# Kernel tuning notes

Hardware: AMD Instinct MI355X
Metric: run time of the kernel (lower is better)

Reference implementation:

```python
import jax, jax.numpy as jnp
import numpy as np

B, T, C = 8, 1024, 576
NH, NKV = 9, 3          # query heads, kv heads
HD = C // NH            # 64 head dim
KVC = C // NKV          # 192 kv proj width
N_REP = NH // NKV       # 3


def setup_inputs() -> dict:
    key = jax.random.key(0)
    ks = jax.random.split(key, 9)
    s = 0.02
    return {
        "x": jax.random.normal(ks[0], (B, T, C), jnp.float32),
        "Wq": jax.random.normal(ks[1], (C, C), jnp.float32) * s,
        "bq": jax.random.normal(ks[2], (C,), jnp.float32) * s,
        "Wk": jax.random.normal(ks[3], (C, KVC), jnp.float32) * s,
        "bk": jax.random.normal(ks[4], (KVC,), jnp.float32) * s,
        "Wv": jax.random.normal(ks[5], (C, KVC), jnp.float32) * s,
        "bv": jax.random.normal(ks[6], (KVC,), jnp.float32) * s,
        "Wo": jax.random.normal(ks[7], (C, C), jnp.float32) * s,
        "bo": jax.random.normal(ks[8], (C,), jnp.float32) * s,
    }


def reference(x, Wq, bq, Wk, bk, Wv, bv, Wo, bo):
    Bx, Tx, Cx = x.shape
    q = x @ Wq + bq                                # [B,T,C]
    k = x @ Wk + bk                                # [B,T,KVC]
    v = x @ Wv + bv
    # split heads: q -> [B,NH,T,HD]; k,v -> [B,NKV,T,HD]
    q = q.reshape(Bx, Tx, NH, HD).transpose(0, 2, 1, 3)
    k = k.reshape(Bx, Tx, NKV, HD).transpose(0, 2, 1, 3)
    v = v.reshape(Bx, Tx, NKV, HD).transpose(0, 2, 1, 3)
    # repeat_kv: [B,NKV,T,HD] -> [B,NKV*N_REP,T,HD]
    k = jnp.repeat(k, N_REP, axis=1)
    v = jnp.repeat(v, N_REP, axis=1)
    att = jnp.einsum("bhqd,bhkd->bhqk", q, k) * (1.0 / np.sqrt(HD))
    mask = jnp.tril(jnp.ones((Tx, Tx), bool))
    att = jnp.where(mask, att, -jnp.inf)
    att = jax.nn.softmax(att, axis=-1)
    y = jnp.einsum("bhqk,bhkd->bhqd", att, v)      # [B,NH,T,HD]
    y = y.transpose(0, 2, 1, 3).reshape(Bx, Tx, Cx)
    return y @ Wo + bo
```

## Files before the change

kernel.cpp:

```cpp
#include <hip/hip_runtime.h>
#include <hip/hip_bf16.h>
#include <math.h>

#define B_    8
#define T_    1024
#define C_    576
#define NH_   9
#define NKV_  3
#define HD_   64
#define KVC_  192
#define NREP_ 3
#define NQKV_ 960
#define NTK_  9

typedef __attribute__((ext_vector_type(8))) short bf16x8;
typedef __attribute__((ext_vector_type(4))) float f32x4;
typedef __attribute__((ext_vector_type(4))) int i32x4;

#define MFMA_16x16x32(a, b, c) __builtin_amdgcn_mfma_f32_16x16x32_bf16((a), (b), (c), 0, 0, 0)

__device__ __forceinline__ ushort f2bf(float f) {
  __hip_bfloat16 h = __float2bfloat16(f);
  return *reinterpret_cast<const ushort*>(&h);
}

__device__ __forceinline__ float fexp2(float x) { return __builtin_amdgcn_exp2f(x); }

__device__ __forceinline__ int swz(int row, int col) {
  int byte = (row << 7) + (col << 1);
  return (byte ^ ((row & 7) << 4)) >> 1;
}

__device__ __forceinline__ void gload16(const ushort* g, ushort* l) {
  __builtin_amdgcn_global_load_lds(
      (const __attribute__((address_space(1))) unsigned int*)g,
      (__attribute__((address_space(3))) unsigned int*)l, 16, 0, 0);
}

__device__ __forceinline__ i32x4 packrow(const float* src) {
  const float4 a = *reinterpret_cast<const float4*>(src);
  const float4 b = *reinterpret_cast<const float4*>(src + 4);
  union { ushort u[8]; i32x4 v; } t;
  t.u[0] = f2bf(a.x); t.u[1] = f2bf(a.y); t.u[2] = f2bf(a.z); t.u[3] = f2bf(a.w);
  t.u[4] = f2bf(b.x); t.u[5] = f2bf(b.y); t.u[6] = f2bf(b.z); t.u[7] = f2bf(b.w);
  return t.v;
}

__global__ __launch_bounds__(256) void convert_x_kernel(
    const float* __restrict__ x, ushort* __restrict__ xbt) {
  const int tm = blockIdx.x, tk = blockIdx.y;
  ushort* dst = xbt + ((size_t)tm * NTK_ + tk) * 8192;
  #pragma unroll
  for (int i = 0; i < 4; i++) {
    const int c = threadIdx.x + i * 256;
    const int row = c >> 3, colb = (c & 7) * 8;
    *reinterpret_cast<i32x4*>(&dst[swz(row, colb)]) =
        packrow(x + (size_t)(tm * 128 + row) * C_ + tk * 64 + colb);
  }
}

__global__ __launch_bounds__(256) void convert_w_kernel(
    const float* __restrict__ Wq, const float* __restrict__ Wk,
    const float* __restrict__ Wv, const float* __restrict__ Wo,
    const float* __restrict__ bq, const float* __restrict__ bk,
    const float* __restrict__ bv, const float* __restrict__ bo,
    ushort* __restrict__ wqkvT, ushort* __restrict__ woT, float* __restrict__ bcat) {
  const int tnc = blockIdx.x, tk = blockIdx.y;
  #pragma unroll
  for (int i = 0; i < 2; i++) {
    const int c = threadIdx.x + i * 256;
    const int row = c >> 3, colb = (c & 7) * 8;
    const float* src; int ld; ushort* dst; int ncol;
    if (tnc < 15) {
      const int n = tnc * 64 + row;
      if (n < 576)      { src = Wq; ld = C_;  ncol = n; }
      else if (n < 768) { src = Wk; ld = KVC_; ncol = n - 576; }
      else              { src = Wv; ld = KVC_; ncol = n - 768; }
      dst = wqkvT + ((size_t)tnc * NTK_ + tk) * 4096;
    } else {
      src = Wo; ld = C_; ncol = (tnc - 15) * 64 + row;
      dst = woT + ((size_t)(tnc - 15) * NTK_ + tk) * 4096;
    }
    union { ushort u[8]; i32x4 v; } t;
    #pragma unroll
    for (int e = 0; e < 8; e++)
      t.u[e] = f2bf(src[(size_t)(tk * 64 + colb + e) * ld + ncol]);
    *reinterpret_cast<i32x4*>(&dst[swz(row, colb)]) = t.v;
    if (tk == 0 && (c & 7) == 0) {
      const int n = tnc * 64 + row;
      float bv_;
      if (n < 576)       bv_ = bq[n];
      else if (n < 768)  bv_ = bk[n - 576];
      else if (n < 960)  bv_ = bv[n - 768];
      else               bv_ = bo[n - 960];
      bcat[n] = bv_;
    }
  }
}

template<int MODE>
__global__ __launch_bounds__(256) void gemm_lds_kernel(
    const ushort* __restrict__ At, const ushort* __restrict__ Bt,
    const float* __restrict__ bias, void* __restrict__ Cp,
    ushort* __restrict__ ktv, ushort* __restrict__ vtv, int N) {
  const int nwg = gridDim.x * gridDim.y;
  const int flat = blockIdx.y * gridDim.x + blockIdx.x;
  const int wg = (flat & 7) * (nwg >> 3) + (flat >> 3);
  const int bxs = wg % gridDim.x, bys = wg / gridDim.x;

  __shared__ ushort As[128 * 64];
  __shared__ ushort Bs[64 * 64];
  const int bm = bys * 128, bn = bxs * 64;
  const int tid = threadIdx.x;
  const int wave = tid >> 6, lane = tid & 63;
  const int lg = lane >> 4, ll = lane & 15;
  const int wm = (wave >> 1) * 64, wn = (wave & 1) * 32;
  f32x4 acc[4][2] = {};

  const ushort* abase = At + (size_t)bys * NTK_ * 8192;
  const ushort* bbase = Bt + (size_t)bxs * NTK_ * 4096;

  for (int kt = 0; kt < NTK_; kt++) {
    const ushort* ak = abase + (size_t)kt * 8192;
    const ushort* bk = bbase + (size_t)kt * 4096;
    #pragma unroll
    for (int i = 0; i < 4; i++) {
      const int c0 = (wave << 6) + (i << 8);
      gload16(ak + (size_t)(c0 + lane) * 8, &As[c0 * 8]);
    }
    #pragma unroll
    for (int i = 0; i < 2; i++) {
      const int c0 = (wave << 6) + (i << 8);
      gload16(bk + (size_t)(c0 + lane) * 8, &Bs[c0 * 8]);
    }
    __syncthreads();

    bf16x8 af[4][2], bfr[2][2];
    #pragma unroll
    for (int mt = 0; mt < 4; mt++) {
      af[mt][0] = *reinterpret_cast<const bf16x8*>(&As[swz(wm + mt * 16 + ll, lg * 8)]);
      af[mt][1] = *reinterpret_cast<const bf16x8*>(&As[swz(wm + mt * 16 + ll, 32 + lg * 8)]);
    }
    #pragma unroll
    for (int nt = 0; nt < 2; nt++) {
      bfr[nt][0] = *reinterpret_cast<const bf16x8*>(&Bs[swz(wn + nt * 16 + ll, lg * 8)]);
      bfr[nt][1] = *reinterpret_cast<const bf16x8*>(&Bs[swz(wn + nt * 16 + ll, 32 + lg * 8)]);
    }
    #pragma unroll
    for (int mt = 0; mt < 4; mt++) {
      #pragma unroll
      for (int nt = 0; nt < 2; nt++) {
        acc[mt][nt] = MFMA_16x16x32(af[mt][0], bfr[nt][0], acc[mt][nt]);
        acc[mt][nt] = MFMA_16x16x32(af[mt][1], bfr[nt][1], acc[mt][nt]);
      }
    }
    __syncthreads();
  }

  #pragma unroll
  for (int mt = 0; mt < 4; mt++) {
    #pragma unroll
    for (int nt = 0; nt < 2; nt++) {
      const int col = bn + wn + nt * 16 + ll;
      #pragma unroll
      for (int r = 0; r < 4; r++) {
        const int row = bm + wm + mt * 16 + lg * 4 + r;
        const float val = acc[mt][nt][r] + bias[col];
        if (MODE == 0) {
          ((float*)Cp)[(size_t)row * N + col] = val;
        } else {
          if (col < 576) {
            ((ushort*)Cp)[(size_t)row * C_ + col] = f2bf(val * 0.18033688011112042f);
          } else if (col < 768) {
            const int kvh = (col - 576) >> 6, d = (col - 576) & 63;
            ushort* t = ktv + (((size_t)(row >> 10) * 3 + kvh) * 16 + ((row >> 6) & 15)) * 4096;
            t[swz(row & 63, d)] = f2bf(val);
          } else {
            const int kvh = (col - 768) >> 6, d = (col - 768) & 63;
            ushort* t = vtv + (((size_t)(row >> 10) * 3 + kvh) * 16 + ((row >> 6) & 15)) * 4096;
            t[swz(d, row & 63)] = f2bf(val);
          }
        }
      }
    }
  }
}

__global__ __launch_bounds__(256) void attn_mfma_kernel(
    const ushort* __restrict__ qb, const ushort* __restrict__ ktv,
    const ushort* __restrict__ vtv, ushort* __restrict__ yt) {
  const int qt = 15 - blockIdx.z, h = blockIdx.x, b = blockIdx.y;
  const int kvh = h / NREP_;
  const int tid = threadIdx.x;
  const int wave = tid >> 6, lane = tid & 63;
  const int lg = lane >> 4, ll = lane & 15;
  const int w16 = wave << 4;
  const int qrow0 = qt << 6;
  const int nk = (qt + 2) >> 1;

  __shared__ ushort Ks[2][4096];
  __shared__ ushort Vts[2][4096];
  __shared__ ushort Ps[4][1024];

  const ushort* ktb = ktv + ((size_t)b * 3 + kvh) * 16 * 4096;
  const ushort* vtb = vtv + ((size_t)b * 3 + kvh) * 16 * 4096;

  const ushort* qrow = qb + (size_t)(b * T_ + qrow0 + w16 + ll) * C_ + h * HD_;
  const bf16x8 qa0 = *reinterpret_cast<const bf16x8*>(qrow + lg * 8);
  const bf16x8 qa1 = *reinterpret_cast<const bf16x8*>(qrow + 32 + lg * 8);

  f32x4 o[4] = {};
  float m_i = -INFINITY, l_i = 0.f;

  #pragma unroll 1
  for (int kt = 0; kt < nk; kt++) {
    #pragma unroll
    for (int sub = 0; sub < 2; sub++) {
      const ushort* ks = ktb + (size_t)(2 * kt + sub) * 4096;
      const ushort* vs = vtb + (size_t)(2 * kt + sub) * 4096;
      #pragma unroll
      for (int i = 0; i < 2; i++) {
        const int c0 = (wave << 6) + (i << 8);
        gload16(ks + (size_t)(c0 + lane) * 8, &Ks[sub][c0 * 8]);
        gload16(vs + (size_t)(c0 + lane) * 8, &Vts[sub][c0 * 8]);
      }
    }
    __syncthreads();

    f32x4 s[8];
    #pragma unroll
    for (int kc = 0; kc < 8; kc++) {
      const int sub = kc >> 2, kcl = kc & 3;
      const bf16x8 kb0 = *reinterpret_cast<const bf16x8*>(&Ks[sub][swz(kcl * 16 + ll, lg * 8)]);
      const bf16x8 kb1 = *reinterpret_cast<const bf16x8*>(&Ks[sub][swz(kcl * 16 + ll, 32 + lg * 8)]);
      f32x4 z = {};
      z = MFMA_16x16x32(kb0, qa0, z);
      s[kc] = MFMA_16x16x32(kb1, qa1, z);
    }

    if (kt == nk - 1) {
      const int qg = qrow0 + w16 + ll - (kt << 7);
      #pragma unroll
      for (int kc = 0; kc < 8; kc++)
        #pragma unroll
        for (int r = 0; r < 4; r++)
          if (kc * 16 + lg * 4 + r > qg) s[kc][r] = -INFINITY;
    }

    float mA[8];
    #pragma unroll
    for (int kc = 0; kc < 8; kc++)
      mA[kc] = fmaxf(fmaxf(s[kc][0], s[kc][1]), fmaxf(s[kc][2], s[kc][3]));
    float t0 = fmaxf(fmaxf(fmaxf(mA[0], mA[1]), fmaxf(mA[2], mA[3])),
                     fmaxf(fmaxf(mA[4], mA[5]), fmaxf(mA[6], mA[7])));
    t0 = fmaxf(t0, __shfl_xor(t0, 16));
    t0 = fmaxf(t0, __shfl_xor(t0, 32));
    if (!__all(t0 <= m_i + 11.5415603f)) {
      const float mn = fmaxf(m_i, t0);
      const float al = fexp2(m_i - mn);
      m_i = mn;
      l_i *= al;
      #pragma unroll
      for (int r = 0; r < 4; r++) {
        const float ar = __shfl(al, lg * 4 + r);
        o[0][r] *= ar; o[1][r] *= ar; o[2][r] *= ar; o[3][r] *= ar;
      }
    }

    float rsub[2];
    ushort* Pw = Ps[wave];
    #pragma unroll
    for (int sub = 0; sub < 2; sub++) {
      float rk[4];
      #pragma unroll
      for (int kcl = 0; kcl < 4; kcl++) {
        const int kc = sub * 4 + kcl;
        float p0 = fexp2(s[kc][0] - m_i);
        float p1 = fexp2(s[kc][1] - m_i);
        float p2 = fexp2(s[kc][2] - m_i);
        float p3 = fexp2(s[kc][3] - m_i);
        rk[kcl] = (p0 + p1) + (p2 + p3);
        uint w01 = (uint)f2bf(p0) | ((uint)f2bf(p1) << 16);
        uint w23 = (uint)f2bf(p2) | ((uint)f2bf(p3) << 16);
        *reinterpret_cast<uint*>(&Pw[swz(ll, kcl * 16 + lg * 4)])     = w01;
        *reinterpret_cast<uint*>(&Pw[swz(ll, kcl * 16 + lg * 4 + 2)]) = w23;
      }
      rsub[sub] = (rk[0] + rk[1]) + (rk[2] + rk[3]);
      #pragma unroll
      for (int khl = 0; khl < 2; khl++) {
        const bf16x8 pa = *reinterpret_cast<const bf16x8*>(&Pw[swz(ll, khl * 32 + lg * 8)]);
        #pragma unroll
        for (int d0 = 0; d0 < 4; d0++) {
          const bf16x8 vbr = *reinterpret_cast<const bf16x8*>(&Vts[sub][swz(d0 * 16 + ll, khl * 32 + lg * 8)]);
          o[d0] = MFMA_16x16x32(pa, vbr, o[d0]);
        }
      }
    }
    float rs = rsub[0] + rsub[1];
    rs += __shfl_xor(rs, 16);
    rs += __shfl_xor(rs, 32);
    l_i += rs;

    __syncthreads();
  }

  #pragma unroll
  for (int r = 0; r < 4; r++) {
    const float lr = __shfl(l_i, lg * 4 + r);
    const float inv = 1.f / lr;
    const int rowg = b * T_ + qrow0 + w16 + lg * 4 + r;
    ushort* ybase = yt + ((size_t)(rowg >> 7) * NTK_ + h) * 8192;
    const int lrow = rowg & 127;
    #pragma unroll
    for (int d0 = 0; d0 < 4; d0++) {
      ybase[swz(lrow, d0 * 16 + ll)] = f2bf(o[d0][r] * inv);
    }
  }
}

extern "C" void kernel_launch(void* const* d_in, const int* in_sizes, int n_in,
                              void* d_out, int out_size, void* d_ws, size_t ws_size,
                              hipStream_t stream) {
  const float* x  = (const float*)d_in[0];
  const float* Wq = (const float*)d_in[1];
  const float* bq = (const float*)d_in[2];
  const float* Wk = (const float*)d_in[3];
  const float* bk = (const float*)d_in[4];
  const float* Wv = (const float*)d_in[5];
  const float* bv = (const float*)d_in[6];
  const float* Wo = (const float*)d_in[7];
  const float* bo = (const float*)d_in[8];
  float* out = (float*)d_out;

  const int M = B_ * T_;
  ushort* wqkvT = (ushort*)d_ws;
  ushort* woT   = wqkvT + (size_t)15 * NTK_ * 4096;
  float*  bcat  = (float*)(woT + (size_t)9 * NTK_ * 4096);
  ushort* qb    = (ushort*)(bcat + 1536);
  ushort* ktv   = qb + (size_t)M * C_;
  ushort* vtv   = ktv + (size_t)B_ * NKV_ * 16 * 4096;
  ushort* yt    = vtv + (size_t)B_ * NKV_ * 16 * 4096;
  ushort* xbt   = yt + (size_t)M * C_;

  convert_w_kernel<<<dim3(24, NTK_), 256, 0, stream>>>(Wq, Wk, Wv, Wo, bq, bk, bv, bo,
                                                       wqkvT, woT, bcat);
  convert_x_kernel<<<dim3(M / 128, NTK_), 256, 0, stream>>>(x, xbt);
  gemm_lds_kernel<1><<<dim3(NQKV_ / 64, M / 128), 256, 0, stream>>>(
      xbt, wqkvT, bcat, qb, ktv, vtv, NQKV_);
  attn_mfma_kernel<<<dim3(NH_, B_, 16), 256, 0, stream>>>(qb, ktv, vtv, yt);
  gemm_lds_kernel<0><<<dim3(C_ / 64, M / 128), 256, 0, stream>>>(
      yt, woT, bcat + NQKV_, out, nullptr, nullptr, C_);
}
```

Measured before the change: 72.32 us.

## Split long causal query tiles across two blocks and merge partials

The eight longest causal query tiles (qt 8..15) now have their key range split in half across two blocks each. Each half writes unnormalized fp32 partial outputs plus the running max and sum to a workspace buffer. A new merge kernel combines each pair with log-sum-exp rescaling into the bf16 output. The goal is to balance the causal workload and shorten the critical path of the attention kernel. The cost is an extra kernel launch, fp32 partial traffic, and a dependence on the workspace being large enough.

```diff
diff --git a/kernel.cpp b/kernel.cpp
--- a/kernel.cpp
+++ b/kernel.cpp
@@ -188,15 +188,29 @@
 
 __global__ __launch_bounds__(256) void attn_mfma_kernel(
     const ushort* __restrict__ qb, const ushort* __restrict__ ktv,
-    const ushort* __restrict__ vtv, ushort* __restrict__ yt) {
-  const int qt = 15 - blockIdx.z, h = blockIdx.x, b = blockIdx.y;
+    const ushort* __restrict__ vtv, ushort* __restrict__ yt,
+    float* __restrict__ opart) {
+  const int h = blockIdx.x, b = blockIdx.y, bz = blockIdx.z;
+  int qt, kt0, kt1;
+  bool split;
+  if (bz < 16) {
+    qt = 15 - (bz >> 1);
+    const int nk = (qt + 2) >> 1, cA = (nk + 1) >> 1;
+    kt0 = (bz & 1) ? cA : 0;
+    kt1 = (bz & 1) ? nk : cA;
+    split = true;
+  } else {
+    qt = 23 - bz;
+    kt0 = 0; kt1 = (qt + 2) >> 1;
+    split = false;
+  }
+  const int nk_last = ((qt + 2) >> 1) - 1;
   const int kvh = h / NREP_;
   const int tid = threadIdx.x;
   const int wave = tid >> 6, lane = tid & 63;
   const int lg = lane >> 4, ll = lane & 15;
   const int w16 = wave << 4;
   const int qrow0 = qt << 6;
-  const int nk = (qt + 2) >> 1;
 
   __shared__ ushort Ks[2][4096];
   __shared__ ushort Vts[2][4096];
@@ -213,7 +227,7 @@
   float m_i = -INFINITY, l_i = 0.f;
 
   #pragma unroll 1
-  for (int kt = 0; kt < nk; kt++) {
+  for (int kt = kt0; kt < kt1; kt++) {
     #pragma unroll
     for (int sub = 0; sub < 2; sub++) {
       const ushort* ks = ktb + (size_t)(2 * kt + sub) * 4096;
@@ -238,7 +252,7 @@
       s[kc] = MFMA_16x16x32(kb1, qa1, z);
     }
 
-    if (kt == nk - 1) {
+    if (kt == nk_last) {
       const int qg = qrow0 + w16 + ll - (kt << 7);
       #pragma unroll
       for (int kc = 0; kc < 8; kc++)
@@ -304,17 +318,64 @@
     __syncthreads();
   }
 
+  if (!split) {
+    #pragma unroll
+    for (int r = 0; r < 4; r++) {
+      const float lr = __shfl(l_i, lg * 4 + r);
+      const float inv = 1.f / lr;
+      const int rowg = b * T_ + qrow0 + w16 + lg * 4 + r;
+      ushort* ybase = yt + ((size_t)(rowg >> 7) * NTK_ + h) * 8192;
+      const int lrow = rowg & 127;
+      #pragma unroll
+      for (int d0 = 0; d0 < 4; d0++) {
+        ybase[swz(lrow, d0 * 16 + ll)] = f2bf(o[d0][r] * inv);
+      }
+    }
+  } else {
+    float* op = opart + ((size_t)(h * B_ + b) * 16 + bz) * 4224;
+    #pragma unroll
+    for (int r = 0; r < 4; r++) {
+      const int row = w16 + lg * 4 + r;
+      #pragma unroll
+      for (int d0 = 0; d0 < 4; d0++) {
+        op[row * 64 + d0 * 16 + ll] = o[d0][r];
+      }
+    }
+    if (lg == 0) {
+      op[4096 + w16 + ll] = m_i;
+      op[4160 + w16 + ll] = l_i;
+    }
+  }
+}
+
+__global__ __launch_bounds__(256) void attn_merge_kernel(
+    const float* __restrict__ opart, ushort* __restrict__ yt) {
+  const int h = blockIdx.x, b = blockIdx.y, qt = 8 + blockIdx.z;
+  const int tid = threadIdx.x;
+  const int row = tid >> 2, cb = (tid & 3) * 16;
+  const float* p0 = opart + ((size_t)(h * B_ + b) * 16 + (15 - qt) * 2) * 4224;
+  const float* p1 = p0 + 4224;
+
+  const float m0 = p0[4096 + row], m1 = p1[4096 + row];
+  const float l0 = p0[4160 + row], l1 = p1[4160 + row];
+  const float mf = fmaxf(m0, m1);
+  const float a0 = fexp2(m0 - mf), a1 = fexp2(m1 - mf);
+  const float inv = 1.f / (l0 * a0 + l1 * a1);
+
+  const int rowg = b * T_ + (qt << 6) + row;
+  ushort* ybase = yt + ((size_t)(rowg >> 7) * NTK_ + h) * 8192;
+  const int lrow = rowg & 127;
+
   #pragma unroll
-  for (int r = 0; r < 4; r++) {
-    const float lr = __shfl(l_i, lg * 4 + r);
-    const float inv = 1.f / lr;
-    const int rowg = b * T_ + qrow0 + w16 + lg * 4 + r;
-    ushort* ybase = yt + ((size_t)(rowg >> 7) * NTK_ + h) * 8192;
-    const int lrow = rowg & 127;
-    #pragma unroll
-    for (int d0 = 0; d0 < 4; d0++) {
-      ybase[swz(lrow, d0 * 16 + ll)] = f2bf(o[d0][r] * inv);
-    }
+  for (int half = 0; half < 2; half++) {
+    const int c0 = cb + half * 8;
+    union { ushort u[8]; i32x4 v; } t;
+    #pragma unroll
+    for (int e = 0; e < 8; e++) {
+      const float v = (p0[row * 64 + c0 + e] * a0 + p1[row * 64 + c0 + e] * a1) * inv;
+      t.u[e] = f2bf(v);
+    }
+    *reinterpret_cast<i32x4*>(&ybase[swz(lrow, c0)]) = t.v;
   }
 }
 
@@ -341,13 +402,15 @@
   ushort* vtv   = ktv + (size_t)B_ * NKV_ * 16 * 4096;
   ushort* yt    = vtv + (size_t)B_ * NKV_ * 16 * 4096;
   ushort* xbt   = yt + (size_t)M * C_;
+  float*  opart = (float*)(xbt + (size_t)M * C_);
 
   convert_w_kernel<<<dim3(24, NTK_), 256, 0, stream>>>(Wq, Wk, Wv, Wo, bq, bk, bv, bo,
                                                        wqkvT, woT, bcat);
   convert_x_kernel<<<dim3(M / 128, NTK_), 256, 0, stream>>>(x, xbt);
   gemm_lds_kernel<1><<<dim3(NQKV_ / 64, M / 128), 256, 0, stream>>>(
       xbt, wqkvT, bcat, qb, ktv, vtv, NQKV_);
-  attn_mfma_kernel<<<dim3(NH_, B_, 16), 256, 0, stream>>>(qb, ktv, vtv, yt);
+  attn_mfma_kernel<<<dim3(NH_, B_, 24), 256, 0, stream>>>(qb, ktv, vtv, yt, opart);
+  attn_merge_kernel<<<dim3(NH_, B_, 8), 256, 0, stream>>>(opart, yt);
   gemm_lds_kernel<0><<<dim3(C_ / 64, M / 128), 256, 0, stream>>>(
       yt, woT, bcat + NQKV_, out, nullptr, nullptr, C_);
 }
```

Measured after the change: 77.09 us. +6.6%, slower.

## Double-buffer 64-key K/V tiles with async prefetch in attention loop

Applied to the files above, without the earlier changes.

The attention loop now walks 64-key tiles instead of 128-key pairs. It prefetches the next tile's K and V into the alternate LDS buffer while computing on the current one, using an explicit vmcnt wait and raw s_barrier instead of __syncthreads. The finer tile granularity also skips the fully masked half tile on the causal diagonal. The cost is twice as many loop iterations, which means more barriers and more online-softmax rescale checks per key. There is also some dependence on the vmcnt count matching the number of outstanding loads.

```diff
diff --git a/kernel.cpp b/kernel.cpp
--- a/kernel.cpp
+++ b/kernel.cpp
@@ -196,7 +196,7 @@
   const int lg = lane >> 4, ll = lane & 15;
   const int w16 = wave << 4;
   const int qrow0 = qt << 6;
-  const int nk = (qt + 2) >> 1;
+  const int ntile = qt + 1;
 
   __shared__ ushort Ks[2][4096];
   __shared__ ushort Vts[2][4096];
@@ -212,47 +212,59 @@
   f32x4 o[4] = {};
   float m_i = -INFINITY, l_i = 0.f;
 
+  {
+    const ushort* ks = ktb;
+    const ushort* vs = vtb;
+    #pragma unroll
+    for (int i = 0; i < 2; i++) {
+      const int c0 = (wave << 6) + (i << 8);
+      gload16(ks + (size_t)(c0 + lane) * 8, &Ks[0][c0 * 8]);
+      gload16(vs + (size_t)(c0 + lane) * 8, &Vts[0][c0 * 8]);
+    }
+  }
+
   #pragma unroll 1
-  for (int kt = 0; kt < nk; kt++) {
-    #pragma unroll
-    for (int sub = 0; sub < 2; sub++) {
-      const ushort* ks = ktb + (size_t)(2 * kt + sub) * 4096;
-      const ushort* vs = vtb + (size_t)(2 * kt + sub) * 4096;
+  for (int t = 0; t < ntile; t++) {
+    const int cur = t & 1;
+    if (t + 1 < ntile) {
+      const ushort* ks = ktb + (size_t)(t + 1) * 4096;
+      const ushort* vs = vtb + (size_t)(t + 1) * 4096;
       #pragma unroll
       for (int i = 0; i < 2; i++) {
         const int c0 = (wave << 6) + (i << 8);
-        gload16(ks + (size_t)(c0 + lane) * 8, &Ks[sub][c0 * 8]);
-        gload16(vs + (size_t)(c0 + lane) * 8, &Vts[sub][c0 * 8]);
-      }
-    }
-    __syncthreads();
-
-    f32x4 s[8];
-    #pragma unroll
-    for (int kc = 0; kc < 8; kc++) {
-      const int sub = kc >> 2, kcl = kc & 3;
-      const bf16x8 kb0 = *reinterpret_cast<const bf16x8*>(&Ks[sub][swz(kcl * 16 + ll, lg * 8)]);
-      const bf16x8 kb1 = *reinterpret_cast<const bf16x8*>(&Ks[sub][swz(kcl * 16 + ll, 32 + lg * 8)]);
+        gload16(ks + (size_t)(c0 + lane) * 8, &Ks[cur ^ 1][c0 * 8]);
+        gload16(vs + (size_t)(c0 + lane) * 8, &Vts[cur ^ 1][c0 * 8]);
+      }
+      asm volatile("s_waitcnt vmcnt(4)" ::: "memory");
+    } else {
+      asm volatile("s_waitcnt vmcnt(0)" ::: "memory");
+    }
+    __builtin_amdgcn_s_barrier();
+
+    f32x4 s[4];
+    #pragma unroll
+    for (int kcl = 0; kcl < 4; kcl++) {
+      const bf16x8 kb0 = *reinterpret_cast<const bf16x8*>(&Ks[cur][swz(kcl * 16 + ll, lg * 8)]);
+      const bf16x8 kb1 = *reinterpret_cast<const bf16x8*>(&Ks[cur][swz(kcl * 16 + ll, 32 + lg * 8)]);
       f32x4 z = {};
       z = MFMA_16x16x32(kb0, qa0, z);
-      s[kc] = MFMA_16x16x32(kb1, qa1, z);
-    }
-
-    if (kt == nk - 1) {
-      const int qg = qrow0 + w16 + ll - (kt << 7);
-      #pragma unroll
-      for (int kc = 0; kc < 8; kc++)
+      s[kcl] = MFMA_16x16x32(kb1, qa1, z);
+    }
+
+    if (t == ntile - 1) {
+      const int qg = qrow0 + w16 + ll - (t << 6);
+      #pragma unroll
+      for (int kcl = 0; kcl < 4; kcl++)
         #pragma unroll
         for (int r = 0; r < 4; r++)
-          if (kc * 16 + lg * 4 + r > qg) s[kc][r] = -INFINITY;
-    }
-
-    float mA[8];
-    #pragma unroll
-    for (int kc = 0; kc < 8; kc++)
-      mA[kc] = fmaxf(fmaxf(s[kc][0], s[kc][1]), fmaxf(s[kc][2], s[kc][3]));
-    float t0 = fmaxf(fmaxf(fmaxf(mA[0], mA[1]), fmaxf(mA[2], mA[3])),
-                     fmaxf(fmaxf(mA[4], mA[5]), fmaxf(mA[6], mA[7])));
+          if (kcl * 16 + lg * 4 + r > qg) s[kcl][r] = -INFINITY;
+    }
+
+    float mA[4];
+    #pragma unroll
+    for (int kcl = 0; kcl < 4; kcl++)
+      mA[kcl] = fmaxf(fmaxf(s[kcl][0], s[kcl][1]), fmaxf(s[kcl][2], s[kcl][3]));
+    float t0 = fmaxf(fmaxf(mA[0], mA[1]), fmaxf(mA[2], mA[3]));
     t0 = fmaxf(t0, __shfl_xor(t0, 16));
     t0 = fmaxf(t0, __shfl_xor(t0, 32));
     if (!__all(t0 <= m_i + 11.5415603f)) {
@@ -267,41 +279,35 @@
       }
     }
 
-    float rsub[2];
+    float rk[4];
     ushort* Pw = Ps[wave];
     #pragma unroll
-    for (int sub = 0; sub < 2; sub++) {
-      float rk[4];
-      #pragma unroll
-      for (int kcl = 0; kcl < 4; kcl++) {
-        const int kc = sub * 4 + kcl;
-        float p0 = fexp2(s[kc][0] - m_i);
-        float p1 = fexp2(s[kc][1] - m_i);
-        float p2 = fexp2(s[kc][2] - m_i);
-        float p3 = fexp2(s[kc][3] - m_i);
-        rk[kcl] = (p0 + p1) + (p2 + p3);
-        uint w01 = (uint)f2bf(p0) | ((uint)f2bf(p1) << 16);
-        uint w23 = (uint)f2bf(p2) | ((uint)f2bf(p3) << 16);
-        *reinterpret_cast<uint*>(&Pw[swz(ll, kcl * 16 + lg * 4)])     = w01;
-        *reinterpret_cast<uint*>(&Pw[swz(ll, kcl * 16 + lg * 4 + 2)]) = w23;
-      }
-      rsub[sub] = (rk[0] + rk[1]) + (rk[2] + rk[3]);
-      #pragma unroll
-      for (int khl = 0; khl < 2; khl++) {
-        const bf16x8 pa = *reinterpret_cast<const bf16x8*>(&Pw[swz(ll, khl * 32 + lg * 8)]);
-        #pragma unroll
-        for (int d0 = 0; d0 < 4; d0++) {
-          const bf16x8 vbr = *reinterpret_cast<const bf16x8*>(&Vts[sub][swz(d0 * 16 + ll, khl * 32 + lg * 8)]);
-          o[d0] = MFMA_16x16x32(pa, vbr, o[d0]);
-        }
-      }
-    }
-    float rs = rsub[0] + rsub[1];
+    for (int kcl = 0; kcl < 4; kcl++) {
+      float p0 = fexp2(s[kcl][0] - m_i);
+      float p1 = fexp2(s[kcl][1] - m_i);
+      float p2 = fexp2(s[kcl][2] - m_i);
+      float p3 = fexp2(s[kcl][3] - m_i);
+      rk[kcl] = (p0 + p1) + (p2 + p3);
+      uint w01 = (uint)f2bf(p0) | ((uint)f2bf(p1) << 16);
+      uint w23 = (uint)f2bf(p2) | ((uint)f2bf(p3) << 16);
+      *reinterpret_cast<uint*>(&Pw[swz(ll, kcl * 16 + lg * 4)])     = w01;
+      *reinterpret_cast<uint*>(&Pw[swz(ll, kcl * 16 + lg * 4 + 2)]) = w23;
+    }
+    #pragma unroll
+    for (int khl = 0; khl < 2; khl++) {
+      const bf16x8 pa = *reinterpret_cast<const bf16x8*>(&Pw[swz(ll, khl * 32 + lg * 8)]);
+      #pragma unroll
+      for (int d0 = 0; d0 < 4; d0++) {
+        const bf16x8 vbr = *reinterpret_cast<const bf16x8*>(&Vts[cur][swz(d0 * 16 + ll, khl * 32 + lg * 8)]);
+        o[d0] = MFMA_16x16x32(pa, vbr, o[d0]);
+      }
+    }
+    float rs = (rk[0] + rk[1]) + (rk[2] + rk[3]);
     rs += __shfl_xor(rs, 16);
     rs += __shfl_xor(rs, 32);
     l_i += rs;
 
-    __syncthreads();
+    __builtin_amdgcn_s_barrier();
   }
 
   #pragma unroll
```

Measured after the change: 70.65 us (median of 2 runs). -2.3%, faster.
